# Performance work log

Hardware: AMD Instinct MI355X
Metric: run time of the kernel (lower is better)

The kernel has to match this reference:

```python
import jax, jax.numpy as jnp
import numpy as np

ALPHA = 0.2       # LeakyReLU negative slope
LN_EPS = 1e-5     # nn.LayerNorm default eps
MASK_VAL = -1e9   # masked_fill value in original


def setup_inputs() -> dict:
    key = jax.random.key(0)
    ks = jax.random.split(key, 8)
    B, N, D_IN, D_OUT = 1, 1024, 64, 64
    def lin(k, fan_in, shape):
        return jax.random.normal(k, shape, dtype=jnp.float32) / np.sqrt(fan_in)
    return {
        "h": jax.random.normal(ks[0], (B, N, D_IN), dtype=jnp.float32),
        "adj": jax.random.randint(ks[1], (B, N, N), 0, 2, dtype=jnp.int32),
        "W": lin(ks[2], D_IN, (D_IN, D_OUT)),                 # W (no bias)
        "attn_w1": lin(ks[3], 3 * D_OUT, (3 * D_OUT, D_OUT)),  # attention_mlp layer 1
        "attn_b1": jnp.zeros((D_OUT,), jnp.float32),
        "attn_w2": lin(ks[4], D_OUT, (D_OUT, 1)),              # attention_mlp layer 2
        "attn_b2": jnp.zeros((1,), jnp.float32),
        "edge_w": lin(ks[5], 2 * D_IN, (2 * D_IN, D_OUT)),     # edge_encoder linear
        "edge_b": jnp.zeros((D_OUT,), jnp.float32),
        "ln_g": jnp.ones((D_OUT,), jnp.float32),
        "ln_b": jnp.zeros((D_OUT,), jnp.float32),
    }


def reference(h, adj, W, attn_w1, attn_b1, attn_w2, attn_b2, edge_w, edge_b, ln_g, ln_b):
    # Eval mode: dropout is identity. in_features == out_features -> residual_proj is None.
    d_in = h.shape[-1]
    d = W.shape[1]
    Wh = h @ W  # [b, n, d]

    # Split concat-linears into per-block matmuls (math identical to cat+Linear,
    # avoids materializing the [b,n,n,3d] and [b,n,n,2d] concat tensors).
    E_i, E_j = edge_w[:d_in], edge_w[d_in:]
    ei = h @ E_i  # [b, n, d]
    ej = h @ E_j
    # edge_encoder(cat(h_i, h_j)) -> [b, n, n, d]
    edge = jax.nn.leaky_relu(ei[:, :, None, :] + ej[:, None, :, :] + edge_b, ALPHA)

    A_i, A_j, A_e = attn_w1[:d], attn_w1[d:2 * d], attn_w1[2 * d:]
    pre = ((Wh @ A_i)[:, :, None, :] + (Wh @ A_j)[:, None, :, :]
           + edge @ A_e + attn_b1)                      # [b, n, n, d]
    hid = jax.nn.leaky_relu(pre, ALPHA)
    e = jnp.squeeze(hid @ attn_w2, -1) + attn_b2[0]     # [b, n, n]

    e = jnp.where(adj == 0, MASK_VAL, e)
    attention = jax.nn.softmax(e, axis=-1)              # [b, n, n]

    h_prime = attention @ Wh + h                        # residual (in == out)

    mu = jnp.mean(h_prime, axis=-1, keepdims=True)
    var = jnp.mean(jnp.square(h_prime - mu), axis=-1, keepdims=True)
    out = (h_prime - mu) / jnp.sqrt(var + LN_EPS) * ln_g + ln_b
    return out
```

## Files before the change

### kernel.cpp

```cpp
#include <hip/hip_runtime.h>
#include <math.h>

#define N 1024
#define D 64
#define ALPHA 0.2f
#define LN_EPS 1e-5f
#define MASK_VAL -1000000000.0f

typedef __attribute__((ext_vector_type(8))) short bf16x8;
typedef __attribute__((ext_vector_type(4))) float f32x4;

__device__ __forceinline__ float leaky(float x) { return fmaxf(x, ALPHA * x); }

__device__ __forceinline__ unsigned f2bf_u(float f) {
    unsigned u = __builtin_bit_cast(unsigned, f);
    u += 0x7fffu + ((u >> 16) & 1u);
    return u >> 16;
}
__device__ __forceinline__ short f2bf(float f) { return (short)f2bf_u(f); }

__device__ __forceinline__ unsigned abs_rne_pair(float x, float y) {
    unsigned ux = __builtin_bit_cast(unsigned, x) & 0x7fffffffu;
    unsigned uy = __builtin_bit_cast(unsigned, y) & 0x7fffffffu;
    ux += 0x7fffu + ((ux >> 16) & 1u);
    uy += 0x7fffu + ((uy >> 16) & 1u);
    return __builtin_amdgcn_perm(uy, ux, 0x07060302);
}

union BF8 { bf16x8 v; unsigned u[4]; };

__global__ __launch_bounds__(256) void gat_precompute(
    const float* __restrict__ h, const float* __restrict__ W,
    const float* __restrict__ attn_w1, const float* __restrict__ attn_b1,
    const float* __restrict__ edge_w, const float* __restrict__ edge_b,
    float* __restrict__ Wh, float* __restrict__ ejB, float* __restrict__ ei_o,
    float* __restrict__ ajT, float* __restrict__ aiF)
{
    const int tid = threadIdx.x;
    const int r = tid >> 6;
    const int k = tid & 63;
    const int i = blockIdx.x * 4 + r;
    const float* __restrict__ Ae = attn_w1 + 2 * D * D;
    __shared__ float hrow[4][D], whrow[4][D], eirow[4][D], ejrow[4][D];

    hrow[r][k] = h[(size_t)i * D + k];
    __syncthreads();

    float wh = 0.f, vei = 0.f, vej = 0.f;
    #pragma unroll 8
    for (int m = 0; m < D; ++m) {
        float hm = hrow[r][m];
        wh  = fmaf(hm, W[m * D + k], wh);
        vei = fmaf(hm, edge_w[m * D + k], vei);
        vej = fmaf(hm, edge_w[(m + D) * D + k], vej);
    }
    vej += edge_b[k];
    Wh[(size_t)i * D + k]   = wh;
    ei_o[(size_t)i * D + k] = vei;
    ejB[(size_t)i * D + k]  = vej;
    whrow[r][k] = wh; eirow[r][k] = vei; ejrow[r][k] = vej;
    __syncthreads();

    float vai = 0.f, vaj = 0.f, vea = 0.f, veb = 0.f;
    #pragma unroll 8
    for (int m = 0; m < D; ++m) {
        float wm = whrow[r][m];
        float aem = Ae[m * D + k];
        vai = fmaf(wm, attn_w1[m * D + k], vai);
        vaj = fmaf(wm, attn_w1[(m + D) * D + k], vaj);
        vea = fmaf(ejrow[r][m], aem, vea);
        veb = fmaf(eirow[r][m], aem, veb);
    }
    ajT[(size_t)k * N + i]  = vaj + 0.6f * vea;
    aiF[(size_t)i * D + k]  = vai + attn_b1[k] + 0.6f * veb;
}

__global__ __launch_bounds__(256) void gat_scores(
    const float* __restrict__ ejB, const float* __restrict__ ajT,
    const float* __restrict__ ei, const float* __restrict__ aiF,
    const float* __restrict__ attn_w1, const float* __restrict__ attn_w2,
    const float* __restrict__ attn_b2, const int* __restrict__ adj,
    float* __restrict__ e_out)
{
    const int tid  = threadIdx.x;
    const int lane = tid & 63;
    const int wid  = tid >> 6;
    const int nloc = lane & 15;
    const int quad = lane >> 4;
    const int i0   = (blockIdx.x >> 4) * 16;
    const int j16  = (blockIdx.x & 15) * 64 + wid * 16;
    const float* __restrict__ Ae = attn_w1 + 2 * D * D;

    __shared__ __align__(16) float sv[16][D];
    __shared__ float av[16][D];
    {
        float* svf = &sv[0][0];
        float* avf = &av[0][0];
        #pragma unroll
        for (int c = 0; c < 4; ++c) {
            svf[c * 256 + tid] = ei[(size_t)i0 * D + c * 256 + tid];
            avf[c * 256 + tid] = aiF[(size_t)i0 * D + c * 256 + tid];
        }
    }
    __syncthreads();

    bf16x8 Bf[2][4];
    #pragma unroll
    for (int kt = 0; kt < 2; ++kt)
        #pragma unroll
        for (int ot = 0; ot < 4; ++ot)
            #pragma unroll
            for (int idx = 0; idx < 8; ++idx) {
                int k = kt * 32 + quad * 8 + idx;
                Bf[kt][ot][idx] = f2bf(0.4f * Ae[(size_t)k * D + ot * 16 + nloc]);
            }

    float w2l[4];
    #pragma unroll
    for (int ot = 0; ot < 4; ++ot) w2l[ot] = attn_w2[ot * 16 + nloc];
    const float b2 = attn_b2[0];
    const int k0 = quad * 8;

    const float* __restrict__ ejr = ejB + (size_t)(j16 + nloc) * D;
    const f32x4 ev0 = *(const f32x4*)(ejr + k0);
    const f32x4 ev1 = *(const f32x4*)(ejr + k0 + 4);
    const f32x4 ev2 = *(const f32x4*)(ejr + 32 + k0);
    const f32x4 ev3 = *(const f32x4*)(ejr + 32 + k0 + 4);
    f32x4 ajv[4];
    #pragma unroll
    for (int ot = 0; ot < 4; ++ot)
        ajv[ot] = *(const f32x4*)(ajT + (size_t)(ot * 16 + nloc) * N + j16 + quad * 4);

    #pragma unroll 4
    for (int ii = 0; ii < 16; ++ii) {
        const f32x4 s0 = *(const f32x4*)(&sv[ii][k0]);
        const f32x4 s1 = *(const f32x4*)(&sv[ii][k0 + 4]);
        const f32x4 s2 = *(const f32x4*)(&sv[ii][32 + k0]);
        const f32x4 s3 = *(const f32x4*)(&sv[ii][32 + k0 + 4]);

        BF8 af0, af1;
        f32x4 t;
        t = ev0 + s0; af0.u[0] = abs_rne_pair(t.x, t.y); af0.u[1] = abs_rne_pair(t.z, t.w);
        t = ev1 + s1; af0.u[2] = abs_rne_pair(t.x, t.y); af0.u[3] = abs_rne_pair(t.z, t.w);
        t = ev2 + s2; af1.u[0] = abs_rne_pair(t.x, t.y); af1.u[1] = abs_rne_pair(t.z, t.w);
        t = ev3 + s3; af1.u[2] = abs_rne_pair(t.x, t.y); af1.u[3] = abs_rne_pair(t.z, t.w);

        f32x4 acc[4];
        #pragma unroll
        for (int ot = 0; ot < 4; ++ot) {
            acc[ot] = __builtin_amdgcn_mfma_f32_16x16x32_bf16(af0.v, Bf[0][ot], ajv[ot], 0, 0, 0);
            acc[ot] = __builtin_amdgcn_mfma_f32_16x16x32_bf16(af1.v, Bf[1][ot], acc[ot], 0, 0, 0);
        }

        float part[4] = {0.f, 0.f, 0.f, 0.f};
        #pragma unroll
        for (int ot = 0; ot < 4; ++ot) {
            const float avli = av[ii][ot * 16 + nloc];
            #pragma unroll
            for (int r = 0; r < 4; ++r)
                part[r] = fmaf(leaky(acc[ot][r] + avli), w2l[ot], part[r]);
        }
        #pragma unroll
        for (int r = 0; r < 4; ++r) {
            float v = part[r];
            v += __shfl_xor(v, 1, 64);
            v += __shfl_xor(v, 2, 64);
            v += __shfl_xor(v, 4, 64);
            v += __shfl_xor(v, 8, 64);
            part[r] = v;
        }
        if (nloc == 0) {
            const int jr = j16 + quad * 4;
            const size_t base = (size_t)(i0 + ii) * N + jr;
            const int4 am = *(const int4*)(adj + base);
            f32x4 res;
            res.x = am.x ? part[0] + b2 : MASK_VAL;
            res.y = am.y ? part[1] + b2 : MASK_VAL;
            res.z = am.z ? part[2] + b2 : MASK_VAL;
            res.w = am.w ? part[3] + b2 : MASK_VAL;
            *(f32x4*)(e_out + base) = res;
        }
    }
}

__global__ __launch_bounds__(256) void gat_softagg(
    const float* __restrict__ e_in, const float* __restrict__ Wh,
    const float* __restrict__ h, const float* __restrict__ ln_g,
    const float* __restrict__ ln_b, float* __restrict__ out)
{
    const int tid  = threadIdx.x;
    const int lane = tid & 63;
    const int wid  = tid >> 6;
    const int i0   = blockIdx.x * 2;
    const int r    = wid >> 1;
    const int half = wid & 1;

    __shared__ float p[2][N];
    __shared__ float wred[4][2];
    __shared__ float red[4][2][D];

    {
        const float* __restrict__ erow = e_in + (size_t)(i0 + r) * N;
        float m = -INFINITY;
        #pragma unroll
        for (int c = 0; c < 8; ++c) {
            int j = half * 512 + c * 64 + lane;
            float v = erow[j];
            p[r][j] = v;
            m = fmaxf(m, v);
        }
        #pragma unroll
        for (int off = 32; off >= 1; off >>= 1) m = fmaxf(m, __shfl_xor(m, off, 64));
        if (lane == 0) wred[wid][0] = m;
    }
    __syncthreads();
    {
        float m = fmaxf(wred[r * 2][0], wred[r * 2 + 1][0]);
        float s = 0.f;
        #pragma unroll
        for (int c = 0; c < 8; ++c) {
            int j = half * 512 + c * 64 + lane;
            float pv = __expf(p[r][j] - m);
            p[r][j] = pv;
            s += pv;
        }
        #pragma unroll
        for (int off = 32; off >= 1; off >>= 1) s += __shfl_xor(s, off, 64);
        if (lane == 0) wred[wid][1] = s;
    }
    __syncthreads();

    {
        const int k = lane, g = wid;
        float hp0 = 0.f, hp1 = 0.f;
        #pragma unroll 8
        for (int jj = 0; jj < 256; ++jj) {
            const int j = g * 256 + jj;
            const float whv = Wh[(size_t)j * D + k];
            hp0 = fmaf(p[0][j], whv, hp0);
            hp1 = fmaf(p[1][j], whv, hp1);
        }
        red[g][0][k] = hp0;
        red[g][1][k] = hp1;
    }
    __syncthreads();

    if (wid < 2) {
        const int rr = wid;
        const float inv_s = 1.f / (wred[rr * 2][1] + wred[rr * 2 + 1][1]);
        float v = (red[0][rr][lane] + red[1][rr][lane] +
                   red[2][rr][lane] + red[3][rr][lane]) * inv_s
                  + h[(size_t)(i0 + rr) * D + lane];
        float mu = v;
        #pragma unroll
        for (int off = 32; off >= 1; off >>= 1) mu += __shfl_xor(mu, off, 64);
        mu *= (1.f / D);
        float d = v - mu;
        float var = d * d;
        #pragma unroll
        for (int off = 32; off >= 1; off >>= 1) var += __shfl_xor(var, off, 64);
        var *= (1.f / D);
        out[(size_t)(i0 + rr) * D + lane] = d * rsqrtf(var + LN_EPS) * ln_g[lane] + ln_b[lane];
    }
}

extern "C" void kernel_launch(void* const* d_in, const int* in_sizes, int n_in,
                              void* d_out, int out_size, void* d_ws, size_t ws_size,
                              hipStream_t stream) {
    const float* h       = (const float*)d_in[0];
    const int*   adj     = (const int*)  d_in[1];
    const float* W       = (const float*)d_in[2];
    const float* attn_w1 = (const float*)d_in[3];
    const float* attn_b1 = (const float*)d_in[4];
    const float* attn_w2 = (const float*)d_in[5];
    const float* attn_b2 = (const float*)d_in[6];
    const float* edge_w  = (const float*)d_in[7];
    const float* edge_b  = (const float*)d_in[8];
    const float* ln_g    = (const float*)d_in[9];
    const float* ln_b    = (const float*)d_in[10];
    float* out = (float*)d_out;

    float* ws   = (float*)d_ws;
    float* Wh   = ws + 0 * (N * D);
    float* ejB  = ws + 1 * (N * D);
    float* ei_w = ws + 2 * (N * D);
    float* ajT  = ws + 3 * (N * D);
    float* aiF  = ws + 4 * (N * D);
    float* e    = ws + 5 * (N * D);

    gat_precompute<<<N / 4, 256, 0, stream>>>(h, W, attn_w1, attn_b1, edge_w, edge_b,
                                              Wh, ejB, ei_w, ajT, aiF);
    gat_scores<<<(N / 16) * 16, 256, 0, stream>>>(ejB, ajT, ei_w, aiF,
                                                  attn_w1, attn_w2, attn_b2, adj, e);
    gat_softagg<<<N / 2, 256, 0, stream>>>(e, Wh, h, ln_g, ln_b, out);
}
```

Measured before the change: 127.2 us.

## Swap MFMA operands so output features land in accumulator rows, shrinking reduction

The MFMA operands in the score kernel are swapped so each lane's accumulator holds four output features for one j column rather than four j rows for one feature. The w2 dot product can then run as vectorised f32x4 math with two cross-lane shuffles instead of four 4-step shuffle reductions. The aj bias is now stored row-major instead of transposed so it matches the new accumulator layout, and vector loads of av and w2 replace scalar loads. The store becomes 16 scalar writes per wave instead of 4-wide vector stores, so the final store is less coalesced.

Measured after the change: 125.7 us. About the same (-1.1%).

```diff
diff --git a/kernel.cpp b/kernel.cpp
--- a/kernel.cpp
+++ b/kernel.cpp
@@ -27,6 +27,10 @@
     return __builtin_amdgcn_perm(uy, ux, 0x07060302);
 }
 
+__device__ __forceinline__ f32x4 leaky4(f32x4 v) {
+    return __builtin_elementwise_max(v, v * ALPHA);
+}
+
 union BF8 { bf16x8 v; unsigned u[4]; };
 
 __global__ __launch_bounds__(256) void gat_precompute(
@@ -34,7 +38,7 @@
     const float* __restrict__ attn_w1, const float* __restrict__ attn_b1,
     const float* __restrict__ edge_w, const float* __restrict__ edge_b,
     float* __restrict__ Wh, float* __restrict__ ejB, float* __restrict__ ei_o,
-    float* __restrict__ ajT, float* __restrict__ aiF)
+    float* __restrict__ ajF, float* __restrict__ aiF)
 {
     const int tid = threadIdx.x;
     const int r = tid >> 6;
@@ -71,12 +75,12 @@
         vea = fmaf(ejrow[r][m], aem, vea);
         veb = fmaf(eirow[r][m], aem, veb);
     }
-    ajT[(size_t)k * N + i]  = vaj + 0.6f * vea;
-    aiF[(size_t)i * D + k]  = vai + attn_b1[k] + 0.6f * veb;
+    ajF[(size_t)i * D + k] = vaj + 0.6f * vea;
+    aiF[(size_t)i * D + k] = vai + attn_b1[k] + 0.6f * veb;
 }
 
 __global__ __launch_bounds__(256) void gat_scores(
-    const float* __restrict__ ejB, const float* __restrict__ ajT,
+    const float* __restrict__ ejB, const float* __restrict__ ajF,
     const float* __restrict__ ei, const float* __restrict__ aiF,
     const float* __restrict__ attn_w1, const float* __restrict__ attn_w2,
     const float* __restrict__ attn_b2, const int* __restrict__ adj,
@@ -92,7 +96,7 @@
     const float* __restrict__ Ae = attn_w1 + 2 * D * D;
 
     __shared__ __align__(16) float sv[16][D];
-    __shared__ float av[16][D];
+    __shared__ __align__(16) float av[16][D];
     {
         float* svf = &sv[0][0];
         float* avf = &av[0][0];
@@ -115,9 +119,10 @@
                 Bf[kt][ot][idx] = f2bf(0.4f * Ae[(size_t)k * D + ot * 16 + nloc]);
             }
 
-    float w2l[4];
+    f32x4 w2l[4];
     #pragma unroll
-    for (int ot = 0; ot < 4; ++ot) w2l[ot] = attn_w2[ot * 16 + nloc];
+    for (int ot = 0; ot < 4; ++ot)
+        w2l[ot] = *(const f32x4*)(attn_w2 + ot * 16 + quad * 4);
     const float b2 = attn_b2[0];
     const int k0 = quad * 8;
 
@@ -126,10 +131,11 @@
     const f32x4 ev1 = *(const f32x4*)(ejr + k0 + 4);
     const f32x4 ev2 = *(const f32x4*)(ejr + 32 + k0);
     const f32x4 ev3 = *(const f32x4*)(ejr + 32 + k0 + 4);
+    const float* __restrict__ ajr = ajF + (size_t)(j16 + nloc) * D;
     f32x4 ajv[4];
     #pragma unroll
     for (int ot = 0; ot < 4; ++ot)
-        ajv[ot] = *(const f32x4*)(ajT + (size_t)(ot * 16 + nloc) * N + j16 + quad * 4);
+        ajv[ot] = *(const f32x4*)(ajr + ot * 16 + quad * 4);
 
     #pragma unroll 4
     for (int ii = 0; ii < 16; ++ii) {
@@ -148,37 +154,23 @@
         f32x4 acc[4];
         #pragma unroll
         for (int ot = 0; ot < 4; ++ot) {
-            acc[ot] = __builtin_amdgcn_mfma_f32_16x16x32_bf16(af0.v, Bf[0][ot], ajv[ot], 0, 0, 0);
-            acc[ot] = __builtin_amdgcn_mfma_f32_16x16x32_bf16(af1.v, Bf[1][ot], acc[ot], 0, 0, 0);
-        }
-
-        float part[4] = {0.f, 0.f, 0.f, 0.f};
+            acc[ot] = __builtin_amdgcn_mfma_f32_16x16x32_bf16(Bf[0][ot], af0.v, ajv[ot], 0, 0, 0);
+            acc[ot] = __builtin_amdgcn_mfma_f32_16x16x32_bf16(Bf[1][ot], af1.v, acc[ot], 0, 0, 0);
+        }
+
+        f32x4 e4 = {0.f, 0.f, 0.f, 0.f};
         #pragma unroll
         for (int ot = 0; ot < 4; ++ot) {
-            const float avli = av[ii][ot * 16 + nloc];
-            #pragma unroll
-            for (int r = 0; r < 4; ++r)
-                part[r] = fmaf(leaky(acc[ot][r] + avli), w2l[ot], part[r]);
-        }
-        #pragma unroll
-        for (int r = 0; r < 4; ++r) {
-            float v = part[r];
-            v += __shfl_xor(v, 1, 64);
-            v += __shfl_xor(v, 2, 64);
-            v += __shfl_xor(v, 4, 64);
-            v += __shfl_xor(v, 8, 64);
-            part[r] = v;
-        }
-        if (nloc == 0) {
-            const int jr = j16 + quad * 4;
-            const size_t base = (size_t)(i0 + ii) * N + jr;
-            const int4 am = *(const int4*)(adj + base);
-            f32x4 res;
-            res.x = am.x ? part[0] + b2 : MASK_VAL;
-            res.y = am.y ? part[1] + b2 : MASK_VAL;
-            res.z = am.z ? part[2] + b2 : MASK_VAL;
-            res.w = am.w ? part[3] + b2 : MASK_VAL;
-            *(f32x4*)(e_out + base) = res;
+            const f32x4 avl = *(const f32x4*)(&av[ii][ot * 16 + quad * 4]);
+            e4 += leaky4(acc[ot] + avl) * w2l[ot];
+        }
+        float e = (e4.x + e4.y) + (e4.z + e4.w);
+        e += __shfl_xor(e, 16, 64);
+        e += __shfl_xor(e, 32, 64);
+
+        if (lane < 16) {
+            const size_t idx = (size_t)(i0 + ii) * N + j16 + lane;
+            e_out[idx] = adj[idx] ? (e + b2) : MASK_VAL;
         }
     }
 }
@@ -284,13 +276,13 @@
     float* Wh   = ws + 0 * (N * D);
     float* ejB  = ws + 1 * (N * D);
     float* ei_w = ws + 2 * (N * D);
-    float* ajT  = ws + 3 * (N * D);
+    float* ajF  = ws + 3 * (N * D);
     float* aiF  = ws + 4 * (N * D);
     float* e    = ws + 5 * (N * D);
 
     gat_precompute<<<N / 4, 256, 0, stream>>>(h, W, attn_w1, attn_b1, edge_w, edge_b,
-                                              Wh, ejB, ei_w, ajT, aiF);
-    gat_scores<<<(N / 16) * 16, 256, 0, stream>>>(ejB, ajT, ei_w, aiF,
+                                              Wh, ejB, ei_w, ajF, aiF);
+    gat_scores<<<(N / 16) * 16, 256, 0, stream>>>(ejB, ajF, ei_w, aiF,
                                                   attn_w1, attn_w2, attn_b2, adj, e);
     gat_softagg<<<N / 2, 256, 0, stream>>>(e, Wh, h, ln_g, ln_b, out);
 }
```
